# Kernel tuning notes

Measured on AMD Instinct MI355X. Metric: run time of the kernel, lower is better.

The kernel has to match this reference:

```python
import jax, jax.numpy as jnp
import numpy as np

TAU = 1.0
PAD_IDX = 0
EOS_IDX = 3
NEG = -10000000.0

B, T, H, E, V, BN = 256, 256, 1024, 512, 32000, 512


def setup_inputs() -> dict:
    key = jax.random.key(0)
    ks = jax.random.split(key, 30)
    s = lambda *sh: 0.02
    inp = {}
    inp['input_ids'] = jax.random.randint(ks[0], (B,), 0, V)
    inp['prediction'] = jax.random.normal(ks[1], (B, V), jnp.float32)
    inp['context'] = jax.random.normal(ks[2], (B, T, 2 * H), jnp.float32)
    inp['h0'] = jax.random.normal(ks[3], (2, B, H), jnp.float32)
    inp['mask'] = jax.random.randint(ks[4], (B, 8), 0, V)
    # parameters
    inp['embedding'] = jax.random.normal(ks[5], (V, E), jnp.float32) * 0.02
    inp['ge1_w'] = jax.random.normal(ks[6], (E, E), jnp.float32) * 0.02
    inp['ge1_b'] = jnp.zeros((E,), jnp.float32)
    inp['ge2_w'] = jax.random.normal(ks[7], (E, E), jnp.float32) * 0.02
    inp['ge2_b'] = jnp.zeros((E,), jnp.float32)
    inp['att_we'] = jax.random.normal(ks[8], (2 * H, H), jnp.float32) * 0.02
    inp['att_wd'] = jax.random.normal(ks[9], (H, H), jnp.float32) * 0.02
    inp['att_v'] = jax.random.normal(ks[10], (H,), jnp.float32) * 0.02
    in0 = 2 * H + E
    inp['wih0'] = jax.random.normal(ks[11], (3 * H, in0), jnp.float32) * 0.02
    inp['whh0'] = jax.random.normal(ks[12], (3 * H, H), jnp.float32) * 0.02
    inp['bih0'] = jnp.zeros((3 * H,), jnp.float32)
    inp['bhh0'] = jnp.zeros((3 * H,), jnp.float32)
    inp['wih1'] = jax.random.normal(ks[13], (3 * H, H), jnp.float32) * 0.02
    inp['whh1'] = jax.random.normal(ks[14], (3 * H, H), jnp.float32) * 0.02
    inp['bih1'] = jnp.zeros((3 * H,), jnp.float32)
    inp['bhh1'] = jnp.zeros((3 * H,), jnp.float32)
    inp['bn0_w'] = jax.random.normal(ks[15], (3 * H + E, BN), jnp.float32) * 0.02
    inp['bn0_b'] = jnp.zeros((BN,), jnp.float32)
    inp['bn1_w'] = jax.random.normal(ks[16], (BN, V), jnp.float32) * 0.02
    inp['bn1_b'] = jnp.zeros((V,), jnp.float32)
    return inp


def _gru_cell(x, h, wih, whh, bih, bhh):
    gi = x @ wih.T + bih  # [B, 3H]
    gh = h @ whh.T + bhh
    gi_r, gi_z, gi_n = jnp.split(gi, 3, axis=1)
    gh_r, gh_z, gh_n = jnp.split(gh, 3, axis=1)
    r = jax.nn.sigmoid(gi_r + gh_r)
    z = jax.nn.sigmoid(gi_z + gh_z)
    n = jnp.tanh(gi_n + r * gh_n)
    return (1.0 - z) * n + z * h


def _forward(input_ids, prediction, context, h0, mask, embedding,
             ge1_w, ge1_b, ge2_w, ge2_b, att_we, att_wd, att_v,
             wih0, whh0, bih0, bhh0, wih1, whh1, bih1, bhh1,
             bn0_w, bn0_b, bn1_w, bn1_b):
    embs = embedding[input_ids]  # [B, E]
    # global embedding gate
    probs = jax.nn.softmax(prediction / TAU, axis=1)  # [B, V]
    emb_avg = probs @ embedding  # [B, E]
    Hg = jax.nn.sigmoid(embs @ ge1_w + ge1_b + emb_avg @ ge2_w + ge2_b)
    embs = Hg * embs + (1.0 - Hg) * emb_avg
    # bahdanau attention with query = top-layer hidden
    q = h0[-1]  # [B, H]
    scores = jnp.tanh(context @ att_we + (q @ att_wd)[:, None, :]) @ att_v  # [B, T]
    attn = jax.nn.softmax(scores, axis=1)
    c_t = jnp.einsum('bt,btd->bd', attn, context)  # [B, 2H]
    rnn_in = jnp.concatenate([embs, c_t], axis=1)  # [B, E+2H]
    h1_0 = _gru_cell(rnn_in, h0[0], wih0, whh0, bih0, bhh0)
    h1_1 = _gru_cell(h1_0, h0[1], wih1, whh1, bih1, bhh1)
    output = h1_1
    h1 = jnp.stack([h1_0, h1_1])
    b0 = jnp.tanh(jnp.concatenate([output, c_t, embs], axis=1) @ bn0_w + bn0_b)
    pred = b0 @ bn1_w + bn1_b  # [B, V]
    # masked scatter: forbid already-generated tokens, but keep PAD/EOS columns
    pad_col = pred[:, PAD_IDX]
    eos_col = pred[:, EOS_IDX]
    rows = jnp.arange(pred.shape[0])
    pred = pred.at[rows[:, None], mask].set(NEG)
    pred = pred.at[:, PAD_IDX].set(pad_col)
    pred = pred.at[:, EOS_IDX].set(eos_col)
    return pred, h1, attn


def reference(input_ids, prediction, context, h0, mask, embedding,
              ge1_w, ge1_b, ge2_w, ge2_b, att_we, att_wd, att_v,
              wih0, whh0, bih0, bhh0, wih1, whh1, bih1, bhh1,
              bn0_w, bn0_b, bn1_w, bn1_b):
    return _forward(input_ids, prediction, context, h0, mask, embedding,
                    ge1_w, ge1_b, ge2_w, ge2_b, att_we, att_wd, att_v,
                    wih0, whh0, bih0, bhh0, wih1, whh1, bih1, bhh1,
                    bn0_w, bn0_b, bn1_w, bn1_b)
```

## Files before the change

kernel.cpp:

```cpp
#include <hip/hip_runtime.h>
#include <hip/hip_bf16.h>


typedef unsigned short u16;
typedef unsigned int u32;
typedef float f32x4 __attribute__((ext_vector_type(4)));
typedef u32 u32x4 __attribute__((ext_vector_type(4)));
typedef __bf16 bf16x8 __attribute__((ext_vector_type(8)));
typedef short s16x8 __attribute__((ext_vector_type(8)));

__device__ __forceinline__ u16 f2bf(float x) {
  u32 u = __float_as_uint(x);
  u += 0x7fffu + ((u >> 16) & 1u);
  return (u16)(u >> 16);
}
__device__ __forceinline__ u32 pack2(float a, float b) {
  return (u32)f2bf(a) | ((u32)f2bf(b) << 16);
}
__device__ __forceinline__ u32 cvt2(float a, float b) {
  union { __bf16 h[2]; u32 w; } u;
  u.h[0] = (__bf16)a; u.h[1] = (__bf16)b;
  return u.w;
}
__device__ __forceinline__ float bf2f(u16 v) {
  return __uint_as_float((u32)v << 16);
}
__device__ __forceinline__ f32x4 mfma_bf16(s16x8 a, s16x8 b, f32x4 c) {
  union { s16x8 s; bf16x8 b; } ua, ub;
  ua.s = a; ub.s = b;
  return __builtin_amdgcn_mfma_f32_16x16x32_bf16(ua.b, ub.b, c, 0, 0, 0);
}
__device__ __forceinline__ void gll16(const void* g, void* l) {
  __builtin_amdgcn_global_load_lds((__attribute__((address_space(1))) void*)g,
                                   (__attribute__((address_space(3))) void*)l,
                                   16, 0, 0);
}
__device__ __forceinline__ float sigf(float x) { return 1.0f / (1.0f + __expf(-x)); }

__global__ __launch_bounds__(256) void k_cvt8(const float* __restrict__ s,
                                              u16* __restrict__ d)
{
  size_t i = ((size_t)blockIdx.x * 256 + threadIdx.x) * 8;
  const size_t stride = (size_t)gridDim.x * 2048;
  for (; i < 134217728ull; i += stride) {
    float4 a = *(const float4*)(s + i);
    float4 b = *(const float4*)(s + i + 4);
    u32x4 w = {cvt2(a.x, a.y), cvt2(a.z, a.w), cvt2(b.x, b.y), cvt2(b.z, b.w)};
    *(u32x4*)(d + i) = w;
  }
}

__global__ __launch_bounds__(512, 4) void k_scores_bf(
    const u16* __restrict__ A, const u16* __restrict__ weT,
    const float* __restrict__ qd, const float* __restrict__ att_v,
    float* __restrict__ scores)
{
  __shared__ u16 As[2][4096];
  __shared__ u16 Bs[2][8192];

  const int tid = threadIdx.x;
  const int lane = tid & 63, wid = tid >> 6;
  const int l15 = lane & 15, lg = lane >> 4;
  const int wm = wid >> 2, wn = wid & 3;
  const int n0 = blockIdx.x * 256;
  const int m0 = blockIdx.y * 128;
  const int b = blockIdx.y >> 1;

  const int sslot = ((lane & 3) ^ ((lane >> 3) & 3)) * 8;
  const size_t asrc = (size_t)(m0 + wid * 16 + (lane >> 2)) * 2048 + sslot;
  size_t bsrc[2];
#pragma unroll
  for (int i = 0; i < 2; ++i)
    bsrc[i] = (size_t)(n0 + (wid * 2 + i) * 16 + (lane >> 2)) * 2048 + sslot;

  const int rslot = (lg ^ ((l15 >> 1) & 3)) * 8;
  int aoff[4], boff[4];
#pragma unroll
  for (int mf = 0; mf < 4; ++mf) aoff[mf] = (wm * 64 + mf * 16 + l15) * 32 + rslot;
#pragma unroll
  for (int nf = 0; nf < 4; ++nf) boff[nf] = (wn * 64 + nf * 16 + l15) * 32 + rslot;

  f32x4 acc[4][4];
#pragma unroll
  for (int mf = 0; mf < 4; ++mf)
#pragma unroll
    for (int nf = 0; nf < 4; ++nf) acc[mf][nf] = (f32x4){0.f, 0.f, 0.f, 0.f};

  {
    gll16(A + asrc, &As[0][wid * 512]);
#pragma unroll
    for (int i = 0; i < 2; ++i)
      gll16(weT + bsrc[i], &Bs[0][(wid * 2 + i) * 512]);
  }
  __syncthreads();

  for (int kt = 0; kt < 64; ++kt) {
    const int cur = kt & 1, nxt = cur ^ 1;
    if (kt < 63) {
      gll16(A + asrc + (size_t)(kt + 1) * 32, &As[nxt][wid * 512]);
#pragma unroll
      for (int i = 0; i < 2; ++i)
        gll16(weT + bsrc[i] + (size_t)(kt + 1) * 32, &Bs[nxt][(wid * 2 + i) * 512]);
    }
    s16x8 af[4], bf[4];
#pragma unroll
    for (int mf = 0; mf < 4; ++mf) af[mf] = *(const s16x8*)(&As[cur][0] + aoff[mf]);
#pragma unroll
    for (int nf = 0; nf < 4; ++nf) bf[nf] = *(const s16x8*)(&Bs[cur][0] + boff[nf]);
    __builtin_amdgcn_s_setprio(1);
#pragma unroll
    for (int nf = 0; nf < 4; ++nf)
#pragma unroll
      for (int mf = 0; mf < 4; ++mf)
        acc[mf][nf] = mfma_bf16(af[mf], bf[nf], acc[mf][nf]);
    __builtin_amdgcn_s_setprio(0);
    __syncthreads();
  }

  float rp[4][4] = {{0.f, 0.f, 0.f, 0.f}, {0.f, 0.f, 0.f, 0.f},
                    {0.f, 0.f, 0.f, 0.f}, {0.f, 0.f, 0.f, 0.f}};
#pragma unroll
  for (int nf = 0; nf < 4; ++nf) {
    int col = n0 + wn * 64 + nf * 16 + l15;
    float qv = qd[(size_t)b * 1024 + col];
    float vv = att_v[col];
#pragma unroll
    for (int mf = 0; mf < 4; ++mf)
#pragma unroll
      for (int e = 0; e < 4; ++e)
        rp[mf][e] += tanhf(acc[mf][nf][e] + qv) * vv;
  }
#pragma unroll
  for (int d = 1; d < 16; d <<= 1)
#pragma unroll
    for (int mf = 0; mf < 4; ++mf)
#pragma unroll
      for (int e = 0; e < 4; ++e)
        rp[mf][e] += __shfl_xor(rp[mf][e], d);
  if (l15 == 0) {
#pragma unroll
    for (int mf = 0; mf < 4; ++mf)
#pragma unroll
      for (int e = 0; e < 4; ++e)
        atomicAdd(&scores[(size_t)m0 + wm * 64 + mf * 16 + lg * 4 + e], rp[mf][e]);
  }
}

__global__ __launch_bounds__(256, 3) void k_scores(
    const float* __restrict__ ctx, const u16* __restrict__ weT,
    const float* __restrict__ qd, const float* __restrict__ att_v,
    float* __restrict__ scores)
{
  __shared__ u16 As[2][4096];
  __shared__ u16 Bs[2][4096];

  const int tid = threadIdx.x;
  const int lane = tid & 63, wid = tid >> 6;
  const int l15 = lane & 15, lg = lane >> 4;
  const int wm = wid >> 1, wn = wid & 1;
  const int n0 = blockIdx.x * 128;
  const int m0 = blockIdx.y * 128;
  const int b = blockIdx.y >> 1;

  const int r0 = tid >> 3, c4 = tid & 7;
  const float* actx = ctx + (size_t)(m0 + r0) * 2048 + c4 * 4;
  const int awoff = r0 * 32 + c4 * 4;

  size_t bsrc[2];
#pragma unroll
  for (int i = 0; i < 2; ++i)
    bsrc[i] = (size_t)(n0 + (wid * 2 + i) * 16 + (lane >> 2)) * 2048 + (size_t)(lane & 3) * 8;

  int aoff[4], boff[4];
#pragma unroll
  for (int mf = 0; mf < 4; ++mf) aoff[mf] = (wm * 64 + mf * 16 + l15) * 32 + lg * 8;
#pragma unroll
  for (int nf = 0; nf < 4; ++nf) boff[nf] = (wn * 64 + nf * 16 + l15) * 32 + lg * 8;

  f32x4 acc[4][4];
#pragma unroll
  for (int mf = 0; mf < 4; ++mf)
#pragma unroll
    for (int nf = 0; nf < 4; ++nf) acc[mf][nf] = (f32x4){0.f, 0.f, 0.f, 0.f};

  {
#pragma unroll
    for (int i = 0; i < 2; ++i)
      gll16(weT + bsrc[i], &Bs[0][(wid * 2 + i) * 512]);
#pragma unroll
    for (int j = 0; j < 4; ++j) {
      float4 av = *(const float4*)(actx + (size_t)(j * 32) * 2048);
      u32* w = (u32*)&As[0][awoff + j * 1024];
      w[0] = cvt2(av.x, av.y); w[1] = cvt2(av.z, av.w);
    }
  }
  __syncthreads();

  for (int kt = 0; kt < 64; ++kt) {
    const int cur = kt & 1, nxt = cur ^ 1;
    const bool pf = (kt < 63);
    float4 av[4];
    if (pf) {
#pragma unroll
      for (int i = 0; i < 2; ++i)
        gll16(weT + bsrc[i] + (size_t)(kt + 1) * 32, &Bs[nxt][(wid * 2 + i) * 512]);
#pragma unroll
      for (int j = 0; j < 4; ++j)
        av[j] = *(const float4*)(actx + (size_t)(j * 32) * 2048 + (kt + 1) * 32);
    }
    s16x8 af[4], bf[4];
#pragma unroll
    for (int mf = 0; mf < 4; ++mf) af[mf] = *(const s16x8*)(&As[cur][0] + aoff[mf]);
#pragma unroll
    for (int nf = 0; nf < 4; ++nf) bf[nf] = *(const s16x8*)(&Bs[cur][0] + boff[nf]);
#pragma unroll
    for (int nf = 0; nf < 4; ++nf)
#pragma unroll
      for (int mf = 0; mf < 4; ++mf)
        acc[mf][nf] = mfma_bf16(af[mf], bf[nf], acc[mf][nf]);
    if (pf) {
#pragma unroll
      for (int j = 0; j < 4; ++j) {
        u32* w = (u32*)&As[nxt][awoff + j * 1024];
        w[0] = cvt2(av[j].x, av[j].y); w[1] = cvt2(av[j].z, av[j].w);
      }
    }
    __syncthreads();
  }

  float rp[4][4] = {{0.f, 0.f, 0.f, 0.f}, {0.f, 0.f, 0.f, 0.f},
                    {0.f, 0.f, 0.f, 0.f}, {0.f, 0.f, 0.f, 0.f}};
#pragma unroll
  for (int nf = 0; nf < 4; ++nf) {
    int col = n0 + wn * 64 + nf * 16 + l15;
    float qv = qd[(size_t)b * 1024 + col];
    float vv = att_v[col];
#pragma unroll
    for (int mf = 0; mf < 4; ++mf)
#pragma unroll
      for (int e = 0; e < 4; ++e)
        rp[mf][e] += tanhf(acc[mf][nf][e] + qv) * vv;
  }
#pragma unroll
  for (int d = 1; d < 16; d <<= 1)
#pragma unroll
    for (int mf = 0; mf < 4; ++mf)
#pragma unroll
      for (int e = 0; e < 4; ++e)
        rp[mf][e] += __shfl_xor(rp[mf][e], d);
  if (l15 == 0) {
#pragma unroll
    for (int mf = 0; mf < 4; ++mf)
#pragma unroll
      for (int e = 0; e < 4; ++e)
        atomicAdd(&scores[(size_t)m0 + wm * 64 + mf * 16 + lg * 4 + e], rp[mf][e]);
  }
}

template <int MODE>
__global__ __launch_bounds__(256, 2) void k_gemm(
    const u16* __restrict__ A, const float* __restrict__ W,
    float* __restrict__ C, const float* __restrict__ bias,
    int N, int K, int ksteps_per, int tot_ksteps, int atomic_mode)
{
  __shared__ u16 As[2][8192];
  __shared__ u16 Bs[2][2048];
  const int tid = threadIdx.x, lane = tid & 63, wid = tid >> 6;
  const int l15 = lane & 15, lg = lane >> 4;
  const int m0 = blockIdx.x * 256;
  const int n0 = blockIdx.y * 64;
  const int kc0 = blockIdx.z * ksteps_per;
  int kcn = tot_ksteps - kc0;
  if (kcn > ksteps_per) kcn = ksteps_per;

  size_t asrc[4];
#pragma unroll
  for (int j = 0; j < 4; ++j)
    asrc[j] = (size_t)(m0 + wid * 64 + j * 16 + (lane >> 2)) * K + (size_t)(lane & 3) * 8;
  int aoff[4], boff[4];
#pragma unroll
  for (int mf = 0; mf < 4; ++mf) aoff[mf] = (wid * 64 + mf * 16 + l15) * 32 + lg * 8;
#pragma unroll
  for (int nf = 0; nf < 4; ++nf) boff[nf] = (nf * 16 + l15) * 32 + lg * 8;

  const int b_row = tid >> 2, b_c8 = tid & 3;
  const int b_kk = tid >> 3, b_c4 = tid & 7;

  f32x4 acc[4][4];
#pragma unroll
  for (int mf = 0; mf < 4; ++mf)
#pragma unroll
    for (int nf = 0; nf < 4; ++nf) acc[mf][nf] = (f32x4){0.f, 0.f, 0.f, 0.f};

  {
#pragma unroll
    for (int j = 0; j < 4; ++j)
      gll16(A + asrc[j] + (size_t)kc0 * 32, &As[0][wid * 2048 + j * 512]);
    if (MODE == 0) {
      const float* p = W + (size_t)(n0 + b_row) * K + (size_t)kc0 * 32 + b_c8 * 8;
      float4 v0 = *(const float4*)p, v1 = *(const float4*)(p + 4);
      u32* w = (u32*)&Bs[0][b_row * 32 + b_c8 * 8];
      w[0] = pack2(v0.x, v0.y); w[1] = pack2(v0.z, v0.w);
      w[2] = pack2(v1.x, v1.y); w[3] = pack2(v1.z, v1.w);
    } else {
      const float* p = W + (size_t)(kc0 * 32 + b_kk) * N + n0 + b_c4 * 4;
      float4 v0 = *(const float4*)p;
      float4 v1 = *(const float4*)(p + 32);
      int r0 = b_c4 * 4, r1 = 32 + b_c4 * 4;
      Bs[0][(r0 + 0) * 32 + b_kk] = f2bf(v0.x);
      Bs[0][(r0 + 1) * 32 + b_kk] = f2bf(v0.y);
      Bs[0][(r0 + 2) * 32 + b_kk] = f2bf(v0.z);
      Bs[0][(r0 + 3) * 32 + b_kk] = f2bf(v0.w);
      Bs[0][(r1 + 0) * 32 + b_kk] = f2bf(v1.x);
      Bs[0][(r1 + 1) * 32 + b_kk] = f2bf(v1.y);
      Bs[0][(r1 + 2) * 32 + b_kk] = f2bf(v1.z);
      Bs[0][(r1 + 3) * 32 + b_kk] = f2bf(v1.w);
    }
  }
  __syncthreads();

  for (int s = 0; s < kcn; ++s) {
    const int cur = s & 1, nxt = cur ^ 1;
    const bool pf = (s + 1 < kcn);
    const int ktn = kc0 + s + 1;
    float4 v0, v1;
    if (pf) {
#pragma unroll
      for (int j = 0; j < 4; ++j)
        gll16(A + asrc[j] + (size_t)ktn * 32, &As[nxt][wid * 2048 + j * 512]);
      if (MODE == 0) {
        const float* p = W + (size_t)(n0 + b_row) * K + (size_t)ktn * 32 + b_c8 * 8;
        v0 = *(const float4*)p; v1 = *(const float4*)(p + 4);
      } else {
        const float* p = W + (size_t)(ktn * 32 + b_kk) * N + n0 + b_c4 * 4;
        v0 = *(const float4*)p;
        v1 = *(const float4*)(p + 32);
      }
    }
    s16x8 af[4], bf[4];
#pragma unroll
    for (int mf = 0; mf < 4; ++mf) af[mf] = *(const s16x8*)(&As[cur][0] + aoff[mf]);
#pragma unroll
    for (int nf = 0; nf < 4; ++nf) bf[nf] = *(const s16x8*)(&Bs[cur][0] + boff[nf]);
#pragma unroll
    for (int nf = 0; nf < 4; ++nf)
#pragma unroll
      for (int mf = 0; mf < 4; ++mf)
        acc[mf][nf] = mfma_bf16(af[mf], bf[nf], acc[mf][nf]);
    if (pf) {
      if (MODE == 0) {
        u32* w = (u32*)&Bs[nxt][b_row * 32 + b_c8 * 8];
        w[0] = pack2(v0.x, v0.y); w[1] = pack2(v0.z, v0.w);
        w[2] = pack2(v1.x, v1.y); w[3] = pack2(v1.z, v1.w);
      } else {
        int r0 = b_c4 * 4, r1 = 32 + b_c4 * 4;
        Bs[nxt][(r0 + 0) * 32 + b_kk] = f2bf(v0.x);
        Bs[nxt][(r0 + 1) * 32 + b_kk] = f2bf(v0.y);
        Bs[nxt][(r0 + 2) * 32 + b_kk] = f2bf(v0.z);
        Bs[nxt][(r0 + 3) * 32 + b_kk] = f2bf(v0.w);
        Bs[nxt][(r1 + 0) * 32 + b_kk] = f2bf(v1.x);
        Bs[nxt][(r1 + 1) * 32 + b_kk] = f2bf(v1.y);
        Bs[nxt][(r1 + 2) * 32 + b_kk] = f2bf(v1.z);
        Bs[nxt][(r1 + 3) * 32 + b_kk] = f2bf(v1.w);
      }
    }
    __syncthreads();
  }

  const size_t Ns = (size_t)N;
#pragma unroll
  for (int mf = 0; mf < 4; ++mf)
#pragma unroll
    for (int nf = 0; nf < 4; ++nf) {
      int col = n0 + nf * 16 + l15;
#pragma unroll
      for (int e = 0; e < 4; ++e) {
        int row = m0 + wid * 64 + mf * 16 + lg * 4 + e;
        float v = acc[mf][nf][e];
        if (atomic_mode) atomicAdd(&C[row * Ns + col], v);
        else C[row * Ns + col] = v + (bias ? bias[col] : 0.0f);
      }
    }
}

__global__ __launch_bounds__(256) void k_twe(const float* __restrict__ we, u16* __restrict__ weT)
{
  __shared__ float t[32][33];
  const int n0 = blockIdx.x * 32, k0 = blockIdx.y * 32;
  const int tid = threadIdx.x;
#pragma unroll
  for (int p = 0; p < 4; ++p) {
    int e = tid + p * 256, r = e >> 5, c = e & 31;
    t[r][c] = we[(size_t)(k0 + r) * 1024 + n0 + c];
  }
  __syncthreads();
#pragma unroll
  for (int p = 0; p < 4; ++p) {
    int e = tid + p * 256, n = e >> 5, k = e & 31;
    weT[(size_t)(n0 + n) * 2048 + k0 + k] = f2bf(t[k][n]);
  }
}

__global__ void k_cast(const float* __restrict__ s, u16* __restrict__ d, int n)
{
  int i = blockIdx.x * 256 + threadIdx.x;
  if (i < n) d[i] = f2bf(s[i]);
}

__global__ void k_gather(const int* __restrict__ ids, const float* __restrict__ emb,
                         float* __restrict__ e0, u16* __restrict__ e0b)
{
  int b = blockIdx.x, tid = threadIdx.x;
  int id = ids[b];
  for (int i = tid; i < 512; i += 256) {
    float v = emb[(size_t)id * 512 + i];
    e0[(size_t)b * 512 + i] = v;
    e0b[(size_t)b * 512 + i] = f2bf(v);
  }
}

__global__ __launch_bounds__(256) void k_softmax_pred(const float* __restrict__ pred,
                                                      u16* __restrict__ probs)
{
  __shared__ float sm[4];
  const int row = blockIdx.x, tid = threadIdx.x;
  const float* x = pred + (size_t)row * 32000;
  float mx = -1e30f;
  for (int i = tid; i < 32000; i += 256) mx = fmaxf(mx, x[i]);
#pragma unroll
  for (int d = 1; d < 64; d <<= 1) mx = fmaxf(mx, __shfl_xor(mx, d));
  if ((tid & 63) == 0) sm[tid >> 6] = mx;
  __syncthreads();
  mx = fmaxf(fmaxf(sm[0], sm[1]), fmaxf(sm[2], sm[3]));
  float s = 0.f;
  for (int i = tid; i < 32000; i += 256) s += __expf(x[i] - mx);
#pragma unroll
  for (int d = 1; d < 64; d <<= 1) s += __shfl_xor(s, d);
  __syncthreads();
  if ((tid & 63) == 0) sm[tid >> 6] = s;
  __syncthreads();
  s = sm[0] + sm[1] + sm[2] + sm[3];
  float inv = 1.0f / s;
  for (int i = tid; i < 32000; i += 256)
    probs[(size_t)row * 32000 + i] = f2bf(__expf(x[i] - mx) * inv);
}

__global__ __launch_bounds__(256) void k_softmax_sc(const float* __restrict__ sc,
                                                    float* __restrict__ attn)
{
  __shared__ float sm[4];
  const int row = blockIdx.x, tid = threadIdx.x;
  float x = sc[(size_t)row * 256 + tid];
  float mx = x;
#pragma unroll
  for (int d = 1; d < 64; d <<= 1) mx = fmaxf(mx, __shfl_xor(mx, d));
  if ((tid & 63) == 0) sm[tid >> 6] = mx;
  __syncthreads();
  mx = fmaxf(fmaxf(sm[0], sm[1]), fmaxf(sm[2], sm[3]));
  float e = __expf(x - mx);
  float s = e;
#pragma unroll
  for (int d = 1; d < 64; d <<= 1) s += __shfl_xor(s, d);
  __syncthreads();
  if ((tid & 63) == 0) sm[tid >> 6] = s;
  __syncthreads();
  s = sm[0] + sm[1] + sm[2] + sm[3];
  attn[(size_t)row * 256 + tid] = e / s;
}

__global__ __launch_bounds__(256) void k_ct_bf(const u16* __restrict__ ctxb,
                                               const float* __restrict__ attn,
                                               float* __restrict__ c_t)
{
  const int b = blockIdx.y;
  const int d0 = blockIdx.x * 512 + threadIdx.x * 2;
  const u16* cp = ctxb + (size_t)b * 524288 + d0;
  const float* ar = attn + (size_t)b * 256;
  float a0 = 0.f, a1 = 0.f;
#pragma unroll 8
  for (int t = 0; t < 256; ++t) {
    float a = ar[t];
    ushort2 v = *(const ushort2*)(cp + (size_t)t * 2048);
    a0 += a * bf2f(v.x); a1 += a * bf2f(v.y);
  }
  float2* o = (float2*)(c_t + (size_t)b * 2048 + d0);
  *o = (float2){a0, a1};
}

__global__ __launch_bounds__(256) void k_ct(const float* __restrict__ ctx,
                                            const float* __restrict__ attn,
                                            float* __restrict__ c_t)
{
  const int b = blockIdx.y;
  const int d0 = blockIdx.x * 512 + threadIdx.x * 2;
  const float2* cp = (const float2*)(ctx + (size_t)b * 524288 + d0);
  const float* ar = attn + (size_t)b * 256;
  float ax = 0.f, ay = 0.f;
#pragma unroll 4
  for (int t = 0; t < 256; ++t) {
    float a = ar[t];
    float2 v = cp[(size_t)t * 1024];
    ax += a * v.x; ay += a * v.y;
  }
  c_t[(size_t)b * 2048 + d0] = ax;
  c_t[(size_t)b * 2048 + d0 + 1] = ay;
}

__global__ void k_gate(const float* __restrict__ gepre, const float* __restrict__ b1,
                       const float* __restrict__ b2, const float* __restrict__ e0,
                       const float* __restrict__ ea, float* __restrict__ embs)
{
  int i = blockIdx.x * 256 + threadIdx.x;
  int nn = i & 511;
  float hg = sigf(gepre[i] + b1[nn] + b2[nn]);
  embs[i] = hg * e0[i] + (1.0f - hg) * ea[i];
}

__global__ void k_cat_rnn(const float* __restrict__ embs, const float* __restrict__ ct,
                          u16* __restrict__ out)
{
  int i = blockIdx.x * 256 + threadIdx.x;
  int m = i / 2560, c = i - m * 2560;
  float v = (c < 512) ? embs[(size_t)m * 512 + c] : ct[(size_t)m * 2048 + (c - 512)];
  out[i] = f2bf(v);
}

__global__ void k_gru(const float* __restrict__ gi, const float* __restrict__ gh,
                      const float* __restrict__ bih, const float* __restrict__ bhh,
                      const float* __restrict__ hprev, float* __restrict__ hout,
                      u16* __restrict__ hout_bf)
{
  int i = blockIdx.x * 256 + threadIdx.x;
  int m = i >> 10, h = i & 1023;
  const float* gim = gi + (size_t)m * 3072;
  const float* ghm = gh + (size_t)m * 3072;
  float r = sigf(gim[h] + bih[h] + ghm[h] + bhh[h]);
  float z = sigf(gim[1024 + h] + bih[1024 + h] + ghm[1024 + h] + bhh[1024 + h]);
  float n = tanhf(gim[2048 + h] + bih[2048 + h] + r * (ghm[2048 + h] + bhh[2048 + h]));
  float hv = (1.0f - z) * n + z * hprev[i];
  hout[i] = hv;
  if (hout_bf) hout_bf[i] = f2bf(hv);
}

__global__ void k_cat_bn0(const float* __restrict__ h11, const float* __restrict__ ct,
                          const float* __restrict__ embs, u16* __restrict__ out)
{
  int i = blockIdx.x * 256 + threadIdx.x;
  int m = i / 3584, c = i - m * 3584;
  float v;
  if (c < 1024) v = h11[(size_t)m * 1024 + c];
  else if (c < 3072) v = ct[(size_t)m * 2048 + (c - 1024)];
  else v = embs[(size_t)m * 512 + (c - 3072)];
  out[i] = f2bf(v);
}

__global__ void k_bn0(const float* __restrict__ pre, const float* __restrict__ bias,
                      u16* __restrict__ b0b)
{
  int i = blockIdx.x * 256 + threadIdx.x;
  int nn = i & 511;
  b0b[i] = f2bf(tanhf(pre[i] + bias[nn]));
}

__global__ void k_mask(const int* __restrict__ mask, float* __restrict__ pred)
{
  int t = blockIdx.x * 256 + threadIdx.x;
  if (t >= 2048) return;
  int b = t >> 3;
  int col = mask[t];
  if (col != 0 && col != 3) pred[(size_t)b * 32000 + col] = -10000000.0f;
}

extern "C" void kernel_launch(void* const* d_in, const int* in_sizes, int n_in,
                              void* d_out, int out_size, void* d_ws, size_t ws_size,
                              hipStream_t stream)
{
  const int*   input_ids = (const int*)d_in[0];
  const float* prediction= (const float*)d_in[1];
  const float* context   = (const float*)d_in[2];
  const float* h0        = (const float*)d_in[3];
  const int*   maskp     = (const int*)d_in[4];
  const float* embedding = (const float*)d_in[5];
  const float* ge1_w = (const float*)d_in[6];
  const float* ge1_b = (const float*)d_in[7];
  const float* ge2_w = (const float*)d_in[8];
  const float* ge2_b = (const float*)d_in[9];
  const float* att_we = (const float*)d_in[10];
  const float* att_wd = (const float*)d_in[11];
  const float* att_v  = (const float*)d_in[12];
  const float* wih0 = (const float*)d_in[13];
  const float* whh0 = (const float*)d_in[14];
  const float* bih0 = (const float*)d_in[15];
  const float* bhh0 = (const float*)d_in[16];
  const float* wih1 = (const float*)d_in[17];
  const float* whh1 = (const float*)d_in[18];
  const float* bih1 = (const float*)d_in[19];
  const float* bhh1 = (const float*)d_in[20];
  const float* bn0_w = (const float*)d_in[21];
  const float* bn0_b = (const float*)d_in[22];
  const float* bn1_w = (const float*)d_in[23];
  const float* bn1_b = (const float*)d_in[24];

  float* out = (float*)d_out;
  float* out_pred = out;
  float* out_h1_0 = out + 8192000;
  float* out_h1_1 = out + 8454144;
  float* out_attn = out + 8716288;

  char* ws = (char*)d_ws;
  float* qd      = (float*)(ws + 0);
  float* emb_avg = (float*)(ws + 1048576);
  float* gepre   = (float*)(ws + 1572864);
  float* gi0     = (float*)(ws + 2097152);
  float* gh0     = (float*)(ws + 5242880);
  float* gi1     = (float*)(ws + 8388608);
  float* gh1     = (float*)(ws + 11534336);
  float* bn0pre  = (float*)(ws + 14680064);
  float* scores  = (float*)(ws + 15204352);
  const size_t MS_BYTES = 15466496;
  float* c_t     = (float*)(ws + 15466496);
  float* embs0   = (float*)(ws + 17563648);
  float* embs    = (float*)(ws + 18087936);
  u16* weT       = (u16*)(ws + 18612224);
  u16* h0_bf     = (u16*)(ws + 22806528);
  u16* embs0_bf  = (u16*)(ws + 23855104);
  u16* probs_bf  = (u16*)(ws + 24117248);
  u16* embavg_bf = (u16*)(ws + 40501248);
  u16* rnnin_bf  = (u16*)(ws + 40763392);
  u16* h1_0_bf   = (u16*)(ws + 42074112);
  u16* bn0in_bf  = (u16*)(ws + 42598400);
  u16* b0_bf     = (u16*)(ws + 44433408);
  u16* ctx_bf    = (u16*)(ws + 44695552);
  const bool big = ws_size >= 44695552ull + 268435456ull;

  (void)in_sizes; (void)n_in; (void)out_size;

  hipMemsetAsync(ws, 0, MS_BYTES, stream);

  if (big) k_cvt8<<<8192, 256, 0, stream>>>(context, ctx_bf);
  k_twe<<<dim3(32, 64), 256, 0, stream>>>(att_we, weT);
  k_cast<<<2048, 256, 0, stream>>>(h0, h0_bf, 524288);
  k_gather<<<256, 256, 0, stream>>>(input_ids, embedding, embs0, embs0_bf);
  k_softmax_pred<<<256, 256, 0, stream>>>(prediction, probs_bf);

  k_gemm<1><<<dim3(1, 16, 8), 256, 0, stream>>>(h0_bf + 262144, att_wd, qd, nullptr,
                                                1024, 1024, 4, 32, 1);
  if (big)
    k_scores_bf<<<dim3(4, 512), 512, 0, stream>>>(ctx_bf, weT, qd, att_v, scores);
  else
    k_scores<<<dim3(8, 512), 256, 0, stream>>>(context, weT, qd, att_v, scores);

  k_gemm<1><<<dim3(1, 8, 50), 256, 0, stream>>>(probs_bf, embedding, emb_avg, nullptr,
                                                512, 32000, 20, 1000, 1);
  k_cast<<<512, 256, 0, stream>>>(emb_avg, embavg_bf, 131072);
  k_gemm<1><<<dim3(1, 8, 4), 256, 0, stream>>>(embs0_bf, ge1_w, gepre, nullptr,
                                               512, 512, 4, 16, 1);
  k_gemm<1><<<dim3(1, 8, 4), 256, 0, stream>>>(embavg_bf, ge2_w, gepre, nullptr,
                                               512, 512, 4, 16, 1);
  k_gate<<<512, 256, 0, stream>>>(gepre, ge1_b, ge2_b, embs0, emb_avg, embs);

  k_softmax_sc<<<256, 256, 0, stream>>>(scores, out_attn);
  if (big)
    k_ct_bf<<<dim3(4, 256), 256, 0, stream>>>(ctx_bf, out_attn, c_t);
  else
    k_ct<<<dim3(4, 256), 256, 0, stream>>>(context, out_attn, c_t);

  k_cat_rnn<<<2560, 256, 0, stream>>>(embs, c_t, rnnin_bf);
  k_gemm<0><<<dim3(1, 48, 5), 256, 0, stream>>>(rnnin_bf, wih0, gi0, nullptr,
                                                3072, 2560, 16, 80, 1);
  k_gemm<0><<<dim3(1, 48, 4), 256, 0, stream>>>(h0_bf, whh0, gh0, nullptr,
                                                3072, 1024, 8, 32, 1);
  k_gru<<<1024, 256, 0, stream>>>(gi0, gh0, bih0, bhh0, h0, out_h1_0, h1_0_bf);
  k_gemm<0><<<dim3(1, 48, 4), 256, 0, stream>>>(h1_0_bf, wih1, gi1, nullptr,
                                                3072, 1024, 8, 32, 1);
  k_gemm<0><<<dim3(1, 48, 4), 256, 0, stream>>>(h0_bf + 262144, whh1, gh1, nullptr,
                                                3072, 1024, 8, 32, 1);
  k_gru<<<1024, 256, 0, stream>>>(gi1, gh1, bih1, bhh1, h0 + 262144, out_h1_1, nullptr);

  k_cat_bn0<<<3584, 256, 0, stream>>>(out_h1_1, c_t, embs, bn0in_bf);
  k_gemm<1><<<dim3(1, 8, 16), 256, 0, stream>>>(bn0in_bf, bn0_w, bn0pre, nullptr,
                                                512, 3584, 7, 112, 1);
  k_bn0<<<512, 256, 0, stream>>>(bn0pre, bn0_b, b0_bf);
  k_gemm<1><<<dim3(1, 500, 1), 256, 0, stream>>>(b0_bf, bn1_w, out_pred, bn1_b,
                                                 32000, 512, 16, 16, 0);
  k_mask<<<8, 256, 0, stream>>>(maskp, out_pred);
}
```

Baseline: 885.2 us.

## Deepen attention GEMM prefetch to two stages and use online softmax

The attention-score GEMM loop now issues global-to-LDS loads two k-tiles ahead. It waits with an explicit vmcnt count and raw barriers instead of a full __syncthreads after each tile, so memory latency can overlap with more MFMA work. Separately, the prediction softmax becomes a single-pass online max/sum with a merged reduction, which removes one full read of each 32000-wide row. The risks are the hand-set vmcnt counts, which must match the number of outstanding loads, and a few extra exp calls per element in the online softmax.

```diff
diff --git a/kernel.cpp b/kernel.cpp
--- a/kernel.cpp
+++ b/kernel.cpp
@@ -91,17 +91,17 @@
 #pragma unroll
     for (int i = 0; i < 2; ++i)
       gll16(weT + bsrc[i], &Bs[0][(wid * 2 + i) * 512]);
-  }
-  __syncthreads();
+    gll16(A + asrc + 32, &As[1][wid * 512]);
+#pragma unroll
+    for (int i = 0; i < 2; ++i)
+      gll16(weT + bsrc[i] + 32, &Bs[1][(wid * 2 + i) * 512]);
+  }
 
   for (int kt = 0; kt < 64; ++kt) {
-    const int cur = kt & 1, nxt = cur ^ 1;
-    if (kt < 63) {
-      gll16(A + asrc + (size_t)(kt + 1) * 32, &As[nxt][wid * 512]);
-#pragma unroll
-      for (int i = 0; i < 2; ++i)
-        gll16(weT + bsrc[i] + (size_t)(kt + 1) * 32, &Bs[nxt][(wid * 2 + i) * 512]);
-    }
+    const int cur = kt & 1;
+    if (kt < 63) asm volatile("s_waitcnt vmcnt(3)" ::: "memory");
+    else         asm volatile("s_waitcnt vmcnt(0)" ::: "memory");
+    __builtin_amdgcn_s_barrier();
     s16x8 af[4], bf[4];
 #pragma unroll
     for (int mf = 0; mf < 4; ++mf) af[mf] = *(const s16x8*)(&As[cur][0] + aoff[mf]);
@@ -114,7 +114,13 @@
       for (int mf = 0; mf < 4; ++mf)
         acc[mf][nf] = mfma_bf16(af[mf], bf[nf], acc[mf][nf]);
     __builtin_amdgcn_s_setprio(0);
-    __syncthreads();
+    __builtin_amdgcn_s_barrier();
+    if (kt + 2 < 64) {
+      gll16(A + asrc + (size_t)(kt + 2) * 32, &As[cur][wid * 512]);
+#pragma unroll
+      for (int i = 0; i < 2; ++i)
+        gll16(weT + bsrc[i] + (size_t)(kt + 2) * 32, &Bs[cur][(wid * 2 + i) * 512]);
+    }
   }
 
   float rp[4][4] = {{0.f, 0.f, 0.f, 0.f}, {0.f, 0.f, 0.f, 0.f},
@@ -422,27 +428,30 @@
 __global__ __launch_bounds__(256) void k_softmax_pred(const float* __restrict__ pred,
                                                       u16* __restrict__ probs)
 {
-  __shared__ float sm[4];
+  __shared__ float smM[4], smS[4];
   const int row = blockIdx.x, tid = threadIdx.x;
   const float* x = pred + (size_t)row * 32000;
-  float mx = -1e30f;
-  for (int i = tid; i < 32000; i += 256) mx = fmaxf(mx, x[i]);
-#pragma unroll
-  for (int d = 1; d < 64; d <<= 1) mx = fmaxf(mx, __shfl_xor(mx, d));
-  if ((tid & 63) == 0) sm[tid >> 6] = mx;
+  float m = -3.0e38f, s = 0.f;
+  for (int i = tid; i < 32000; i += 256) {
+    float v = x[i];
+    if (v > m) { s = s * __expf(m - v) + 1.0f; m = v; }
+    else s += __expf(v - m);
+  }
+#pragma unroll
+  for (int d = 1; d < 64; d <<= 1) {
+    float mo = __shfl_xor(m, d), so = __shfl_xor(s, d);
+    float M = fmaxf(m, mo);
+    s = s * __expf(m - M) + so * __expf(mo - M);
+    m = M;
+  }
+  if ((tid & 63) == 0) { smM[tid >> 6] = m; smS[tid >> 6] = s; }
   __syncthreads();
-  mx = fmaxf(fmaxf(sm[0], sm[1]), fmaxf(sm[2], sm[3]));
-  float s = 0.f;
-  for (int i = tid; i < 32000; i += 256) s += __expf(x[i] - mx);
-#pragma unroll
-  for (int d = 1; d < 64; d <<= 1) s += __shfl_xor(s, d);
-  __syncthreads();
-  if ((tid & 63) == 0) sm[tid >> 6] = s;
-  __syncthreads();
-  s = sm[0] + sm[1] + sm[2] + sm[3];
-  float inv = 1.0f / s;
+  float M4 = fmaxf(fmaxf(smM[0], smM[1]), fmaxf(smM[2], smM[3]));
+  float S4 = smS[0] * __expf(smM[0] - M4) + smS[1] * __expf(smM[1] - M4) +
+             smS[2] * __expf(smM[2] - M4) + smS[3] * __expf(smM[3] - M4);
+  float inv = 1.0f / S4;
   for (int i = tid; i < 32000; i += 256)
-    probs[(size_t)row * 32000 + i] = f2bf(__expf(x[i] - mx) * inv);
+    probs[(size_t)row * 32000 + i] = f2bf(__expf(x[i] - M4) * inv);
 }
 
 __global__ __launch_bounds__(256) void k_softmax_sc(const float* __restrict__ sc,
```

New measurement: 873.2 us. About the same (-1.4%).
